# Optimization experiments

Hardware: AMD Instinct MI355X
Metric: run time of the kernel (lower is better)

Reference implementation:

```python
import jax, jax.numpy as jnp
import numpy as np

B, T, C, H = 4, 1024, 512, 8
HD = C // H
N_NODE, F_DIM, TOTAL_DIM = 64, 8, 16
SCALE = 1.0 / np.sqrt(HD)


def _build_mask():
    # causal tril with every (total_dim-1 mod total_dim)-th COLUMN zeroed
    m = np.tril(np.ones((T, T), dtype=np.float32))
    m[:, TOTAL_DIM - 1::TOTAL_DIM] = 0.0
    return jnp.asarray(m)

MASK = _build_mask()  # (T, T), 1 = keep, 0 = mask


def setup_inputs() -> dict:
    key = jax.random.key(0)
    ks = jax.random.split(key, 12)
    s = 0.02
    return {
        "x": jax.random.normal(ks[0], (B, T, C), dtype=jnp.float32),
        "attn_bias": jax.random.normal(ks[1], (H, N_NODE, N_NODE), dtype=jnp.float32) * 0.1,
        "Wq": jax.random.normal(ks[2], (C, C), dtype=jnp.float32) * s,
        "bq": jax.random.normal(ks[3], (C,), dtype=jnp.float32) * s,
        "Wk": jax.random.normal(ks[4], (C, C), dtype=jnp.float32) * s,
        "bk": jax.random.normal(ks[5], (C,), dtype=jnp.float32) * s,
        "Wv": jax.random.normal(ks[6], (C, C), dtype=jnp.float32) * s,
        "bv": jax.random.normal(ks[7], (C,), dtype=jnp.float32) * s,
        "Wp": jax.random.normal(ks[8], (C, C), dtype=jnp.float32) * s,
        "bp": jax.random.normal(ks[9], (C,), dtype=jnp.float32) * s,
    }


def reference(x, attn_bias, Wq, bq, Wk, bk, Wv, bv, Wp, bp):
    Bx, Tx, Cx = x.shape

    def heads(W, b):  # (B,T,C) -> (B,H,T,HD); torch Linear is x @ W.T + b
        return (x @ W.T + b).reshape(Bx, Tx, H, HD).transpose(0, 2, 1, 3)

    q, k, v = heads(Wq, bq), heads(Wk, bk), heads(Wv, bv)

    # repeat_interleave + repeat expansion == kron(attn_bias, ones(f_dim, f_dim))
    d = N_NODE * F_DIM
    bias = jnp.repeat(jnp.repeat(attn_bias, F_DIM, axis=1), F_DIM, axis=2)  # (H, d, d)
    padded_bias = jnp.zeros((H, Tx, Tx), dtype=x.dtype).at[:, :d, :d].set(bias)

    att = jnp.einsum('bhqd,bhkd->bhqk', q, k) * SCALE + padded_bias[None]
    neg = jnp.asarray(-jnp.inf, dtype=att.dtype)
    att = jnp.where(MASK[None, None, :Tx, :Tx] == 0, neg, att)
    att = jax.nn.softmax(att, axis=-1)

    y = jnp.einsum('bhqk,bhkd->bhqd', att, v)
    y = y.transpose(0, 2, 1, 3).reshape(Bx, Tx, Cx)
    return y @ Wp.T + bp
```

## Files before the change

### kernel.cpp

```cpp
#include <hip/hip_runtime.h>

#define T_SEQ 1024
#define C_DIM 512
#define H_HEADS 8
#define HDIM 64
#define B_BATCH 4
#define M_ROWS (B_BATCH * T_SEQ)
#define NSPLIT_TOT 40

typedef __attribute__((ext_vector_type(8))) short short8;
typedef __attribute__((ext_vector_type(4))) float f32x4;

__device__ __forceinline__ unsigned short f2bf(float f) {
    unsigned u = __builtin_bit_cast(unsigned, f);
    u += 0x7FFFu + ((u >> 16) & 1u);
    return (unsigned short)(u >> 16);
}

__device__ __forceinline__ void gload_lds16(const unsigned short* g, unsigned short* l) {
    __builtin_amdgcn_global_load_lds(
        (const __attribute__((address_space(1))) unsigned int*)(const void*)g,
        (__attribute__((address_space(3))) unsigned int*)(void*)l, 16, 0, 0);
}

__device__ __constant__ unsigned char BX_OF[NSPLIT_TOT] =
    {0,1,2,3,4,4,5,5,6,6,7,7,8,8,8,9,9,9,10,10,10,11,11,11,
     12,12,12,12,13,13,13,13,14,14,14,14,15,15,15,15};
__device__ __constant__ unsigned char SP_OF[NSPLIT_TOT] =
    {0,0,0,0,0,1,0,1,0,1,0,1,0,1,2,0,1,2,0,1,2,0,1,2,
     0,1,2,3,0,1,2,3,0,1,2,3,0,1,2,3};
__device__ __constant__ unsigned char CUM_OF[16] =
    {0,1,2,3,4,6,8,10,12,15,18,21,24,28,32,36};

__global__ __launch_bounds__(256) void cast_all(
    const float* __restrict__ x,
    const float* __restrict__ wq, const float* __restrict__ wk,
    const float* __restrict__ wv, const float* __restrict__ wp,
    unsigned short* __restrict__ xb,
    unsigned short* __restrict__ wqb, unsigned short* __restrict__ wkb,
    unsigned short* __restrict__ wvb, unsigned short* __restrict__ wpb)
{
    const long NX = (long)M_ROWS * C_DIM;
    const long NW = (long)C_DIM * C_DIM;
    long i4 = (long)blockIdx.x * blockDim.x + threadIdx.x;
    long base = i4 * 4;
    const float* src; unsigned short* dst; long off;
    if (base < NX) { src = x; dst = xb; off = base; }
    else {
        long r = base - NX;
        int w = (int)(r >> 18);
        off = r & (NW - 1);
        switch (w) {
            case 0:  src = wq; dst = wqb; break;
            case 1:  src = wk; dst = wkb; break;
            case 2:  src = wv; dst = wvb; break;
            default: src = wp; dst = wpb; break;
        }
    }
    float4 v = *(const float4*)(src + off);
    ushort4 o;
    o.x = f2bf(v.x); o.y = f2bf(v.y); o.z = f2bf(v.z); o.w = f2bf(v.w);
    *(ushort4*)(dst + off) = o;
}

__device__ __forceinline__ void gemm_body(
    const unsigned short* __restrict__ A,
    const unsigned short* __restrict__ W,
    const float* __restrict__ bias,
    unsigned short* __restrict__ Obf,
    float* __restrict__ Of,
    int mode)
{
    __shared__ __align__(16) unsigned short Atile[128 * 64];
    __shared__ __align__(16) unsigned short Btile[128 * 64];

    const int tid  = threadIdx.x;
    const int w    = tid >> 6;
    const int lane = tid & 63;
    const int quad = lane >> 4;
    const int l16  = lane & 15;
    const int m0   = blockIdx.x * 128;
    const int n0   = blockIdx.y * 128;
    const int wr   = 64 * (w >> 1);
    const int wc   = 64 * (w & 1);

    f32x4 acc[4][4] = {};

    const int lr = lane >> 3;
    const int lc = lane & 7;

    for (int k0 = 0; k0 < 512; k0 += 64) {
        __syncthreads();
        for (int i = 0; i < 4; ++i) {
            int r0 = 32 * w + 8 * i;
            int r  = r0 + lr;
            int c  = lc ^ (r & 7);
            gload_lds16(&A[(long)(m0 + r) * 512 + k0 + c * 8], &Atile[r0 * 64]);
            gload_lds16(&W[(long)(n0 + r) * 512 + k0 + c * 8], &Btile[r0 * 64]);
        }
        __syncthreads();

        for (int st = 0; st < 2; ++st) {
            const int pc = ((4 * st + quad) ^ (l16 & 7)) * 8;
            short8 af[4], bf[4];
            for (int i = 0; i < 4; ++i)
                af[i] = *(const short8*)&Atile[(wr + 16 * i + l16) * 64 + pc];
            for (int j = 0; j < 4; ++j)
                bf[j] = *(const short8*)&Btile[(wc + 16 * j + l16) * 64 + pc];
            for (int i = 0; i < 4; ++i)
                for (int j = 0; j < 4; ++j)
                    acc[i][j] = (mode == 1)
                        ? __builtin_amdgcn_mfma_f32_16x16x32_bf16(bf[j], af[i], acc[i][j], 0, 0, 0)
                        : __builtin_amdgcn_mfma_f32_16x16x32_bf16(af[i], bf[j], acc[i][j], 0, 0, 0);
        }
    }

    if (mode == 1) {
        for (int j = 0; j < 4; ++j) {
            for (int reg = 0; reg < 4; ++reg) {
                int n = n0 + wc + 16 * j + 4 * quad + reg;
                int h = n >> 6, hd = n & 63;
                float bv = bias[n];
                for (int i = 0; i < 4; ++i) {
                    int t = m0 + wr + 16 * i + l16;
                    int b = t >> 10, tl = t & 1023;
                    Obf[(((long)(b * H_HEADS + h)) * HDIM + hd) * T_SEQ + tl] =
                        f2bf(acc[i][j][reg] + bv);
                }
            }
        }
    } else {
        for (int j = 0; j < 4; ++j) {
            int col = n0 + wc + 16 * j + l16;
            float bv = bias[col];
            for (int i = 0; i < 4; ++i) {
                for (int reg = 0; reg < 4; ++reg) {
                    int row = m0 + wr + 16 * i + 4 * quad + reg;
                    float v = acc[i][j][reg] + bv;
                    if (mode == 2) {
                        Of[(long)row * 512 + col] = v;
                    } else {
                        int b = row >> 10, t = row & 1023;
                        int h = col >> 6,  hd = col & 63;
                        Obf[(((long)(b * H_HEADS + h)) * T_SEQ + t) * HDIM + hd] = f2bf(v);
                    }
                }
            }
        }
    }
}

__global__ __launch_bounds__(256) void gemm_qkv(
    const unsigned short* __restrict__ A,
    const unsigned short* __restrict__ Wq, const unsigned short* __restrict__ Wk,
    const unsigned short* __restrict__ Wv,
    const float* __restrict__ bq, const float* __restrict__ bk, const float* __restrict__ bv,
    unsigned short* __restrict__ Q, unsigned short* __restrict__ K,
    unsigned short* __restrict__ V)
{
    const unsigned short* W; const float* b; unsigned short* O; int mode;
    if (blockIdx.z == 0)      { W = Wq; b = bq; O = Q; mode = 0; }
    else if (blockIdx.z == 1) { W = Wk; b = bk; O = K; mode = 0; }
    else                      { W = Wv; b = bv; O = V; mode = 1; }
    gemm_body(A, W, b, O, nullptr, mode);
}

__global__ __launch_bounds__(256) void gemm_out_k(
    const unsigned short* __restrict__ A, const unsigned short* __restrict__ W,
    const float* __restrict__ bias, float* __restrict__ O)
{
    gemm_body(A, W, bias, nullptr, O, 2);
}

__global__ __launch_bounds__(256) void attn_split(
    const unsigned short* __restrict__ Q, const unsigned short* __restrict__ K,
    const unsigned short* __restrict__ Vt, const float* __restrict__ attn_bias,
    float* __restrict__ Opart, float* __restrict__ lpart)
{
    __shared__ __align__(16) unsigned short Kl[64 * 72];
    __shared__ __align__(16) unsigned short Vl[64 * 72];
    __shared__ __align__(16) unsigned short Pl[4][16 * 72];
    __shared__ float biasl[8][64];

    const int tid  = threadIdx.x;
    const int w    = tid >> 6;
    const int lane = tid & 63;
    const int quad = lane >> 4;
    const int l16  = lane & 15;
    const int sidx = blockIdx.x;
    const int bh   = blockIdx.y;
    const int h    = bh & 7;
    const int bx   = BX_OF[sidx];
    const int sp   = SP_OF[sidx];
    const int q0   = bx * 64;
    const int kt0  = sp * 4;
    const int kt1  = min(kt0 + 4, bx + 1);
    const bool use_bias = (q0 < 512) && (sp < 2);
    const int brow = 2 * w + (quad >> 1);
    const int bcol0 = 2 * 0 + (l16 >> 3);

    if (use_bias) {
        for (int i = tid; i < 512; i += 256) {
            int nq = (q0 >> 3) + (i >> 6);
            biasl[i >> 6][i & 63] = attn_bias[h * 4096 + nq * 64 + (i & 63)];
        }
    }

    const unsigned short* Qbh = Q  + (long)bh * T_SEQ * HDIM;
    const unsigned short* Kbh = K  + (long)bh * T_SEQ * HDIM;
    const unsigned short* Vbh = Vt + (long)bh * HDIM * T_SEQ;

    short8 qf[2];
    {
        int qr = q0 + 16 * w + l16;
        qf[0] = *(const short8*)&Qbh[(long)qr * HDIM + 8 * quad];
        qf[1] = *(const short8*)&Qbh[(long)qr * HDIM + 32 + 8 * quad];
    }

    f32x4 oacc[4] = {};
    float lrow[4] = {0.f, 0.f, 0.f, 0.f};
    const int qrb = q0 + 16 * w + 4 * quad;
    const bool colkeep = (l16 != 15);

    for (int kt = kt0; kt < kt1; ++kt) {
        const int k0 = kt * 64;
        __syncthreads();
        for (int it = 0; it < 2; ++it) {
            int ch = tid + 256 * it;
            int r = ch >> 3, c8 = ch & 7;
            *(short8*)&Kl[r * 72 + c8 * 8] =
                *(const short8*)&Kbh[(long)(k0 + r) * HDIM + c8 * 8];
            *(short8*)&Vl[r * 72 + c8 * 8] =
                *(const short8*)&Vbh[(long)r * T_SEQ + k0 + c8 * 8];
        }
        __syncthreads();

        f32x4 s[4] = {};
        for (int st = 0; st < 2; ++st) {
            for (int ct = 0; ct < 4; ++ct) {
                short8 bf = *(const short8*)&Kl[(16 * ct + l16) * 72 + 32 * st + 8 * quad];
                s[ct] = __builtin_amdgcn_mfma_f32_16x16x32_bf16(qf[st], bf, s[ct], 0, 0, 0);
            }
        }

        const bool diag = (kt == bx);
        for (int ct = 0; ct < 4; ++ct) {
            int kcol = k0 + 16 * ct + l16;
            float bval = use_bias ? biasl[brow][(k0 >> 3) + 2 * ct + bcol0] : 0.f;
            for (int reg = 0; reg < 4; ++reg) {
                float v = s[ct][reg] * 0.125f + bval;
                bool keep = colkeep && (!diag || (kcol <= qrb + reg));
                float p = keep ? __expf(v) : 0.f;
                lrow[reg] += p;
                Pl[w][(4 * quad + reg) * 72 + 16 * ct + l16] = f2bf(p);
            }
        }

        for (int st = 0; st < 2; ++st) {
            short8 af = *(const short8*)&Pl[w][l16 * 72 + 32 * st + 8 * quad];
            for (int ct = 0; ct < 4; ++ct) {
                short8 bf = *(const short8*)&Vl[(16 * ct + l16) * 72 + 32 * st + 8 * quad];
                oacc[ct] = __builtin_amdgcn_mfma_f32_16x16x32_bf16(af, bf, oacc[ct], 0, 0, 0);
            }
        }
    }

    for (int off = 1; off < 16; off <<= 1)
        for (int reg = 0; reg < 4; ++reg)
            lrow[reg] += __shfl_xor(lrow[reg], off);

    const long p = (long)bh * NSPLIT_TOT + sidx;
    float* Op = Opart + p * 4096;
    for (int ct = 0; ct < 4; ++ct)
        for (int reg = 0; reg < 4; ++reg)
            Op[(16 * w + 4 * quad + reg) * 64 + 16 * ct + l16] = oacc[ct][reg];
    if (l16 == 0) {
        for (int reg = 0; reg < 4; ++reg) {
            int qr = 16 * w + 4 * quad + reg;
            lpart[p * 64 + qr] = lrow[reg];
        }
    }
}

__global__ __launch_bounds__(256) void attn_combine(
    const float* __restrict__ Opart, const float* __restrict__ lpart,
    unsigned short* __restrict__ Y)
{
    const int bx = blockIdx.x, bh = blockIdx.y;
    const int b = bh >> 3, h = bh & 7;
    const int ns = (bx >> 2) + 1;
    const long p0 = (long)bh * NSPLIT_TOT + CUM_OF[bx];
    const int tid = threadIdx.x;
    const int qr = tid >> 2;
    const int hs = (tid & 3) * 16;

    float L = 0.f;
    for (int s = 0; s < ns; ++s) L += lpart[(p0 + s) * 64 + qr];

    float acc[16] = {};
    for (int s = 0; s < ns; ++s) {
        const float4* op = (const float4*)(Opart + (p0 + s) * 4096 + qr * 64 + hs);
        for (int j4 = 0; j4 < 4; ++j4) {
            float4 v = op[j4];
            acc[4 * j4 + 0] += v.x; acc[4 * j4 + 1] += v.y;
            acc[4 * j4 + 2] += v.z; acc[4 * j4 + 3] += v.w;
        }
    }
    float inv = 1.f / L;
    int q = bx * 64 + qr;
    unsigned short* y = Y + ((long)b * T_SEQ + q) * C_DIM + h * HDIM + hs;
    for (int j4 = 0; j4 < 4; ++j4) {
        ushort4 o;
        o.x = f2bf(acc[4 * j4 + 0] * inv); o.y = f2bf(acc[4 * j4 + 1] * inv);
        o.z = f2bf(acc[4 * j4 + 2] * inv); o.w = f2bf(acc[4 * j4 + 3] * inv);
        *(ushort4*)(y + 4 * j4) = o;
    }
}

extern "C" void kernel_launch(void* const* d_in, const int* in_sizes, int n_in,
                              void* d_out, int out_size, void* d_ws, size_t ws_size,
                              hipStream_t stream)
{
    const float* x         = (const float*)d_in[0];
    const float* attn_bias = (const float*)d_in[1];
    const float* Wq = (const float*)d_in[2]; const float* bq = (const float*)d_in[3];
    const float* Wk = (const float*)d_in[4]; const float* bk = (const float*)d_in[5];
    const float* Wv = (const float*)d_in[6]; const float* bv = (const float*)d_in[7];
    const float* Wp = (const float*)d_in[8]; const float* bp = (const float*)d_in[9];
    float* out = (float*)d_out;

    const long NX = (long)M_ROWS * C_DIM;
    const long NW = (long)C_DIM * C_DIM;

    unsigned short* xb  = (unsigned short*)d_ws;
    unsigned short* wqb = xb  + NX;
    unsigned short* wkb = wqb + NW;
    unsigned short* wvb = wkb + NW;
    unsigned short* wpb = wvb + NW;
    unsigned short* Qb  = wpb + NW;
    unsigned short* Kb  = Qb  + NX;
    unsigned short* Vtb = Kb  + NX;
    unsigned short* Yb  = Vtb + NX;
    float* Opart = (float*)(Yb + NX);
    float* lpart = Opart + (long)32 * NSPLIT_TOT * 4096;

    long n4 = (NX + 4 * NW) / 4;
    cast_all<<<dim3((unsigned)(n4 / 256)), 256, 0, stream>>>(
        x, Wq, Wk, Wv, Wp, xb, wqb, wkb, wvb, wpb);

    gemm_qkv<<<dim3(M_ROWS / 128, C_DIM / 128, 3), 256, 0, stream>>>(
        xb, wqb, wkb, wvb, bq, bk, bv, Qb, Kb, Vtb);

    attn_split<<<dim3(NSPLIT_TOT, B_BATCH * H_HEADS), 256, 0, stream>>>(
        Qb, Kb, Vtb, attn_bias, Opart, lpart);

    attn_combine<<<dim3(T_SEQ / 64, B_BATCH * H_HEADS), 256, 0, stream>>>(
        Opart, lpart, Yb);

    gemm_out_k<<<dim3(M_ROWS / 128, C_DIM / 128), 256, 0, stream>>>(
        Yb, wpb, bp, out);
}
```

Before: 134.0 us.

## Load attention K/V tiles via direct-to-LDS with XOR swizzle; store partials in bf16

K and V tiles are now loaded with global_load_lds directly into unpadded shared memory. An XOR swizzle on the column chunk avoids bank conflicts without padding, and the MFMA operand reads use the matching swizzle. The split-K partial outputs are written and read as bf16 instead of fp32, which halves the partial-buffer traffic between attn_split and attn_combine. In exchange, partial sums are rounded to bf16 before combining, which loses some precision.

Result: no change. 133.8 us (-0.1%).

```diff
diff --git a/kernel.cpp b/kernel.cpp
--- a/kernel.cpp
+++ b/kernel.cpp
@@ -15,6 +15,10 @@
     unsigned u = __builtin_bit_cast(unsigned, f);
     u += 0x7FFFu + ((u >> 16) & 1u);
     return (unsigned short)(u >> 16);
+}
+
+__device__ __forceinline__ float bf2f(unsigned short u) {
+    return __builtin_bit_cast(float, (unsigned)u << 16);
 }
 
 __device__ __forceinline__ void gload_lds16(const unsigned short* g, unsigned short* l) {
@@ -175,10 +179,10 @@
 __global__ __launch_bounds__(256) void attn_split(
     const unsigned short* __restrict__ Q, const unsigned short* __restrict__ K,
     const unsigned short* __restrict__ Vt, const float* __restrict__ attn_bias,
-    float* __restrict__ Opart, float* __restrict__ lpart)
-{
-    __shared__ __align__(16) unsigned short Kl[64 * 72];
-    __shared__ __align__(16) unsigned short Vl[64 * 72];
+    unsigned short* __restrict__ Opart, float* __restrict__ lpart)
+{
+    __shared__ __align__(16) unsigned short Kl[64 * 64];
+    __shared__ __align__(16) unsigned short Vl[64 * 64];
     __shared__ __align__(16) unsigned short Pl[4][16 * 72];
     __shared__ float biasl[8][64];
 
@@ -187,6 +191,8 @@
     const int lane = tid & 63;
     const int quad = lane >> 4;
     const int l16  = lane & 15;
+    const int lr   = lane >> 3;
+    const int lc   = lane & 7;
     const int sidx = blockIdx.x;
     const int bh   = blockIdx.y;
     const int h    = bh & 7;
@@ -197,7 +203,7 @@
     const int kt1  = min(kt0 + 4, bx + 1);
     const bool use_bias = (q0 < 512) && (sp < 2);
     const int brow = 2 * w + (quad >> 1);
-    const int bcol0 = 2 * 0 + (l16 >> 3);
+    const int bcol0 = l16 >> 3;
 
     if (use_bias) {
         for (int i = tid; i < 512; i += 256) {
@@ -225,20 +231,20 @@
     for (int kt = kt0; kt < kt1; ++kt) {
         const int k0 = kt * 64;
         __syncthreads();
-        for (int it = 0; it < 2; ++it) {
-            int ch = tid + 256 * it;
-            int r = ch >> 3, c8 = ch & 7;
-            *(short8*)&Kl[r * 72 + c8 * 8] =
-                *(const short8*)&Kbh[(long)(k0 + r) * HDIM + c8 * 8];
-            *(short8*)&Vl[r * 72 + c8 * 8] =
-                *(const short8*)&Vbh[(long)r * T_SEQ + k0 + c8 * 8];
+        for (int i = 0; i < 2; ++i) {
+            int r0 = 16 * w + 8 * i;
+            int r  = r0 + lr;
+            int c  = lc ^ (r & 7);
+            gload_lds16(&Kbh[(long)(k0 + r) * HDIM + c * 8], &Kl[r0 * 64]);
+            gload_lds16(&Vbh[(long)r * T_SEQ + k0 + c * 8], &Vl[r0 * 64]);
         }
         __syncthreads();
 
         f32x4 s[4] = {};
         for (int st = 0; st < 2; ++st) {
+            const int pc = ((4 * st + quad) ^ (l16 & 7)) * 8;
             for (int ct = 0; ct < 4; ++ct) {
-                short8 bf = *(const short8*)&Kl[(16 * ct + l16) * 72 + 32 * st + 8 * quad];
+                short8 bf = *(const short8*)&Kl[(16 * ct + l16) * 64 + pc];
                 s[ct] = __builtin_amdgcn_mfma_f32_16x16x32_bf16(qf[st], bf, s[ct], 0, 0, 0);
             }
         }
@@ -257,9 +263,10 @@
         }
 
         for (int st = 0; st < 2; ++st) {
+            const int pc = ((4 * st + quad) ^ (l16 & 7)) * 8;
             short8 af = *(const short8*)&Pl[w][l16 * 72 + 32 * st + 8 * quad];
             for (int ct = 0; ct < 4; ++ct) {
-                short8 bf = *(const short8*)&Vl[(16 * ct + l16) * 72 + 32 * st + 8 * quad];
+                short8 bf = *(const short8*)&Vl[(16 * ct + l16) * 64 + pc];
                 oacc[ct] = __builtin_amdgcn_mfma_f32_16x16x32_bf16(af, bf, oacc[ct], 0, 0, 0);
             }
         }
@@ -270,10 +277,10 @@
             lrow[reg] += __shfl_xor(lrow[reg], off);
 
     const long p = (long)bh * NSPLIT_TOT + sidx;
-    float* Op = Opart + p * 4096;
+    unsigned short* Op = Opart + p * 4096;
     for (int ct = 0; ct < 4; ++ct)
         for (int reg = 0; reg < 4; ++reg)
-            Op[(16 * w + 4 * quad + reg) * 64 + 16 * ct + l16] = oacc[ct][reg];
+            Op[(16 * w + 4 * quad + reg) * 64 + 16 * ct + l16] = f2bf(oacc[ct][reg]);
     if (l16 == 0) {
         for (int reg = 0; reg < 4; ++reg) {
             int qr = 16 * w + 4 * quad + reg;
@@ -283,7 +290,7 @@
 }
 
 __global__ __launch_bounds__(256) void attn_combine(
-    const float* __restrict__ Opart, const float* __restrict__ lpart,
+    const unsigned short* __restrict__ Opart, const float* __restrict__ lpart,
     unsigned short* __restrict__ Y)
 {
     const int bx = blockIdx.x, bh = blockIdx.y;
@@ -299,11 +306,12 @@
 
     float acc[16] = {};
     for (int s = 0; s < ns; ++s) {
-        const float4* op = (const float4*)(Opart + (p0 + s) * 4096 + qr * 64 + hs);
-        for (int j4 = 0; j4 < 4; ++j4) {
-            float4 v = op[j4];
-            acc[4 * j4 + 0] += v.x; acc[4 * j4 + 1] += v.y;
-            acc[4 * j4 + 2] += v.z; acc[4 * j4 + 3] += v.w;
+        const unsigned short* op = Opart + (p0 + s) * 4096 + qr * 64 + hs;
+        short8 v0 = *(const short8*)op;
+        short8 v1 = *(const short8*)(op + 8);
+        for (int k = 0; k < 8; ++k) {
+            acc[k]     += bf2f((unsigned short)v0[k]);
+            acc[k + 8] += bf2f((unsigned short)v1[k]);
         }
     }
     float inv = 1.f / L;
@@ -341,8 +349,8 @@
     unsigned short* Kb  = Qb  + NX;
     unsigned short* Vtb = Kb  + NX;
     unsigned short* Yb  = Vtb + NX;
-    float* Opart = (float*)(Yb + NX);
-    float* lpart = Opart + (long)32 * NSPLIT_TOT * 4096;
+    unsigned short* Opart = Yb + NX;
+    float* lpart = (float*)(Opart + (long)32 * NSPLIT_TOT * 4096);
 
     long n4 = (NX + 4 * NW) / 4;
     cast_all<<<dim3((unsigned)(n4 / 256)), 256, 0, stream>>>(
```
